# Kernel optimization log

Measured on AMD Instinct MI355X. Metric: run time of the kernel, lower is better.

Reference implementation:

```python
import jax, jax.numpy as jnp
import numpy as np

# Static configuration (mirrors TemporalAugmentation with deterministic choices)
B, T_IN, N, C = 32, 512, 543, 3
SPEED = 1.2                      # fixed draw from speed_range (0.8, 1.2)
NEW_T = int(T_IN / SPEED)        # 426
JITTER_FREQ = max(1, NEW_T // 8) # 53
FRAME_DROP_P = 0.1
JITTER_STD = 0.02
NOISE_STD = 0.01
SPATIAL_STD = 0.005


def linresample(x, out_T):
    """F.interpolate(mode='linear', align_corners=True) along last axis."""
    L = x.shape[-1]
    s = jnp.arange(out_T, dtype=x.dtype) * ((L - 1) / (out_T - 1))
    i0 = jnp.clip(jnp.floor(s).astype(jnp.int32), 0, L - 2)
    frac = s - i0.astype(x.dtype)
    return x[..., i0] * (1 - frac) + x[..., i0 + 1] * frac


def setup_inputs() -> dict:
    key = jax.random.key(0)
    k1, k2, k3, k4, k5 = jax.random.split(key, 5)
    x = jax.random.normal(k1, (B, T_IN, N, C), dtype=jnp.float32)
    mask = jnp.ones((B, T_IN), dtype=bool)
    keep_mask = jax.random.bernoulli(k2, 1.0 - FRAME_DROP_P, (B, NEW_T))
    keep_mask = keep_mask.at[:, 0].set(True).at[:, -1].set(True)
    base_jitter = jax.random.normal(k3, (B, JITTER_FREQ), dtype=jnp.float32)
    noise = jax.random.normal(k4, (B, NEW_T, N, C), dtype=jnp.float32)
    spatial_noise = jax.random.normal(k5, (B, 1, N, C), dtype=jnp.float32)
    return {"x": x, "mask": mask, "keep_mask": keep_mask,
            "base_jitter": base_jitter, "noise": noise,
            "spatial_noise": spatial_noise}


def reference(x, mask, keep_mask, base_jitter, noise, spatial_noise):
    Bb, T, Nn, Cc = x.shape
    # --- speed augment: linear resample time axis T -> NEW_T ---
    xt = jnp.moveaxis(x, 1, -1)                 # (B,N,C,T)
    x = jnp.moveaxis(linresample(xt, NEW_T), -1, 1)  # (B,NEW_T,N,C)
    # nearest resample of validity mask (PyTorch 'nearest': floor(t*in/out))
    nidx = jnp.floor(jnp.arange(NEW_T) * (T / NEW_T)).astype(jnp.int32)
    mask = mask[:, nidx]
    T2 = NEW_T
    # --- frame dropout: replace dropped frames with align_corners linear
    # resample of the kept-frame subsequence (length K) back to T2 ---
    K = keep_mask.sum(axis=1)                   # (B,) kept counts
    ar = jnp.arange(T2)
    # stable order putting kept indices first, in original order
    order = jnp.argsort(jnp.where(keep_mask, ar, T2 + ar), axis=1)  # (B,T2)
    s = ar[None, :].astype(x.dtype) * (K[:, None] - 1).astype(x.dtype) / (T2 - 1)
    r0 = jnp.clip(jnp.floor(s).astype(jnp.int32), 0, (K - 2)[:, None])
    frac = (s - r0.astype(x.dtype))[:, :, None, None]
    bidx = jnp.arange(Bb)[:, None]
    idx0 = jnp.take_along_axis(order, r0, axis=1)
    idx1 = jnp.take_along_axis(order, r0 + 1, axis=1)
    interp = x[bidx, idx0] * (1 - frac) + x[bidx, idx1] * frac
    x = jnp.where(keep_mask[:, :, None, None], x, interp)
    mask = mask & keep_mask
    # --- temporal jitter: scale per-frame velocity by smooth jitter curve ---
    jit = linresample(base_jitter * JITTER_STD, T2)   # (B,T2)
    vel = x[:, 1:] - x[:, :-1]
    x = jnp.concatenate([x[:, :1], x[:, 1:] + vel * jit[:, 1:, None, None]], axis=1)
    # --- coordinate noise + per-landmark spatial noise ---
    x = x + noise * NOISE_STD + spatial_noise * SPATIAL_STD
    return x, mask
```

## Files before the change

kernel.cpp:

```cpp
#include <hip/hip_runtime.h>
#include <stdint.h>

#define B_      32
#define T_IN_   512
#define N_      543
#define C_      3
#define NEW_T_  426
#define JF_     53
#define NC_     (N_*C_)
#define XOUT_   (B_*NEW_T_*NC_)
#define NGROUP_ (XOUT_/4)

#define MODE_INT   0
#define MODE_BYTE  1
#define MODE_FLOAT 2

__device__ __forceinline__ bool read_flag(const void* p, int mode, int idx) {
    if (mode == MODE_BYTE)  return ((const uint8_t*)p)[idx] != 0;
    if (mode == MODE_FLOAT) return ((const float*)p)[idx]   != 0.0f;
    return ((const int*)p)[idx] != 0;
}

__global__ __launch_bounds__(512) void prep_kernel(
    const void* __restrict__ maskp,
    const void* __restrict__ keepp,
    const float* __restrict__ bjit,
    float* __restrict__ out_mask,
    int4*  __restrict__ wsF,
    float4* __restrict__ wsW,
    float* __restrict__ wsJ)
{
    const int b = blockIdx.x;
    const int tid = threadIdx.x;

    __shared__ int flags[6];
    __shared__ int s_mode_mask, s_mode_keep;
    if (tid < 6) flags[tid] = 0;
    __syncthreads();
    if (tid < 64) {
        uint32_t vm = ((const uint32_t*)maskp)[tid];
        uint32_t vk = ((const uint32_t*)keepp)[tid];
        if (vm == 0x3F800000u)      atomicOr(&flags[2], 1);
        else if (vm > 1u)           atomicOr(&flags[1], 1);
        if (vk == 0x3F800000u)      atomicOr(&flags[5], 1);
        else if (vk > 1u)           atomicOr(&flags[4], 1);
    }
    __syncthreads();
    if (tid == 0) {
        s_mode_mask = flags[2] ? MODE_FLOAT : (flags[1] ? MODE_BYTE : MODE_INT);
        s_mode_keep = flags[5] ? MODE_FLOAT : (flags[4] ? MODE_BYTE : MODE_INT);
    }
    __syncthreads();
    const int mmode = s_mode_mask, kmode = s_mode_keep;

    __shared__ int sk[512];
    __shared__ int ps[512];
    __shared__ int kept[NEW_T_];

    int kv = 0;
    if (tid < NEW_T_) kv = read_flag(keepp, kmode, b*NEW_T_ + tid) ? 1 : 0;
    sk[tid] = (tid < NEW_T_) ? kv : 0;
    ps[tid] = sk[tid];
    __syncthreads();
    for (int off = 1; off < 512; off <<= 1) {
        int v = (tid >= off) ? ps[tid - off] : 0;
        __syncthreads();
        ps[tid] += v;
        __syncthreads();
    }
    const int K = ps[NEW_T_ - 1];
    if (tid < NEW_T_ && kv) kept[ps[tid] - 1] = tid;
    __syncthreads();

    if (tid < NEW_T_) {
        const int t = tid;
        const float RATX = (float)(511.0 / 425.0);
        float st = (float)t * RATX;
        int i0 = (int)floorf(st);
        if (i0 < 0) i0 = 0; if (i0 > T_IN_ - 2) i0 = T_IN_ - 2;
        float w = st - (float)i0;

        int4 F; float4 W;
        if (kv) {
            F = make_int4(i0, i0 + 1, 0, 1);
            W = make_float4(1.0f - w, w, 0.0f, 0.0f);
        } else {
            float s = ((float)t * (float)(K - 1)) / 425.0f;
            int r0 = (int)floorf(s);
            if (r0 < 0) r0 = 0; if (r0 > K - 2) r0 = K - 2;
            float f = s - (float)r0;
            int j0 = kept[r0], j1 = kept[r0 + 1];
            float s0 = (float)j0 * RATX;
            int a0 = (int)floorf(s0);
            if (a0 < 0) a0 = 0; if (a0 > T_IN_ - 2) a0 = T_IN_ - 2;
            float w0 = s0 - (float)a0;
            float s1 = (float)j1 * RATX;
            int a1 = (int)floorf(s1);
            if (a1 < 0) a1 = 0; if (a1 > T_IN_ - 2) a1 = T_IN_ - 2;
            float w1 = s1 - (float)a1;
            F = make_int4(a0, a0 + 1, a1, a1 + 1);
            W = make_float4((1.0f - f) * (1.0f - w0), (1.0f - f) * w0,
                            f * (1.0f - w1),          f * w1);
        }
        const int bt = b * NEW_T_ + t;
        wsF[bt] = F;
        wsW[bt] = W;

        const float RATJ = (float)(52.0 / 425.0);
        float sj = (float)t * RATJ;
        int ji = (int)floorf(sj);
        if (ji < 0) ji = 0; if (ji > JF_ - 2) ji = JF_ - 2;
        float jf = sj - (float)ji;
        float b0 = bjit[b*JF_ + ji]     * 0.02f;
        float b1 = bjit[b*JF_ + ji + 1] * 0.02f;
        float jv = b0 * (1.0f - jf) + b1 * jf;
        if (t == 0) jv = 0.0f;
        wsJ[bt] = jv;

        float mn = (float)t * (float)(512.0 / 426.0);
        int nidx = (int)floorf(mn);
        if (nidx > T_IN_ - 1) nidx = T_IN_ - 1;
        bool mo = read_flag(maskp, mmode, b*T_IN_ + nidx) && (kv != 0);
        out_mask[bt] = mo ? 1.0f : 0.0f;
    }
}

__global__ __launch_bounds__(256) void main_kernel(
    const float* __restrict__ x,
    const float* __restrict__ noise,
    const float* __restrict__ spat,
    const int4*  __restrict__ wsF,
    const float4* __restrict__ wsW,
    const float* __restrict__ wsJ,
    float* __restrict__ out)
{
    uint32_t g = blockIdx.x * 256u + threadIdx.x;
    if (g >= (uint32_t)NGROUP_) return;
    uint32_t flat = g * 4u;
    uint32_t bt = flat / (uint32_t)NC_;
    uint32_t e  = flat - bt * (uint32_t)NC_;

    if (e <= (uint32_t)(NC_ - 4)) {
        uint32_t b = bt / (uint32_t)NEW_T_;
        const float* xb = x + (size_t)b * (T_IN_ * NC_);
        int4  F  = wsF[bt];  float4 W  = wsW[bt];
        uint32_t pbt = bt ? bt - 1u : 0u;
        int4  FP = wsF[pbt]; float4 WP = wsW[pbt];
        float jv = wsJ[bt];

        const float* p0 = xb + (uint32_t)F.x * NC_ + e;
        const float* p1 = xb + (uint32_t)F.y * NC_ + e;
        const float* p2 = xb + (uint32_t)F.z * NC_ + e;
        const float* p3 = xb + (uint32_t)F.w * NC_ + e;
        const float* q0 = xb + (uint32_t)FP.x * NC_ + e;
        const float* q1 = xb + (uint32_t)FP.y * NC_ + e;
        const float* q2 = xb + (uint32_t)FP.z * NC_ + e;
        const float* q3 = xb + (uint32_t)FP.w * NC_ + e;

        float4 nz = *(const float4*)(noise + flat);
        const float* sp = spat + b * NC_ + e;

        float r[4];
        #pragma unroll
        for (int i = 0; i < 4; i++) {
            float a  = W.x  * p0[i] + W.y  * p1[i] + W.z  * p2[i] + W.w  * p3[i];
            float ap = WP.x * q0[i] + WP.y * q1[i] + WP.z * q2[i] + WP.w * q3[i];
            float nzv = (i == 0) ? nz.x : (i == 1) ? nz.y : (i == 2) ? nz.z : nz.w;
            r[i] = a + (a - ap) * jv + nzv * 0.01f + sp[i] * 0.005f;
        }
        float4 o; o.x = r[0]; o.y = r[1]; o.z = r[2]; o.w = r[3];
        *(float4*)(out + flat) = o;
    } else {
        #pragma unroll
        for (int i = 0; i < 4; i++) {
            uint32_t fl  = flat + i;
            uint32_t bt2 = fl / (uint32_t)NC_;
            uint32_t e2  = fl - bt2 * (uint32_t)NC_;
            uint32_t b2  = bt2 / (uint32_t)NEW_T_;
            const float* xb = x + (size_t)b2 * (T_IN_ * NC_);
            int4  F  = wsF[bt2];  float4 W  = wsW[bt2];
            uint32_t pbt = bt2 ? bt2 - 1u : 0u;
            int4  FP = wsF[pbt];  float4 WP = wsW[pbt];
            float jv = wsJ[bt2];
            float a  = W.x  * xb[(uint32_t)F.x  * NC_ + e2] + W.y  * xb[(uint32_t)F.y  * NC_ + e2]
                     + W.z  * xb[(uint32_t)F.z  * NC_ + e2] + W.w  * xb[(uint32_t)F.w  * NC_ + e2];
            float ap = WP.x * xb[(uint32_t)FP.x * NC_ + e2] + WP.y * xb[(uint32_t)FP.y * NC_ + e2]
                     + WP.z * xb[(uint32_t)FP.z * NC_ + e2] + WP.w * xb[(uint32_t)FP.w * NC_ + e2];
            out[fl] = a + (a - ap) * jv + noise[fl] * 0.01f + spat[b2 * NC_ + e2] * 0.005f;
        }
    }
}

extern "C" void kernel_launch(void* const* d_in, const int* in_sizes, int n_in,
                              void* d_out, int out_size, void* d_ws, size_t ws_size,
                              hipStream_t stream) {
    const float* x    = (const float*)d_in[0];
    const void*  mask = d_in[1];
    const void*  keep = d_in[2];
    const float* bjit = (const float*)d_in[3];
    const float* noise = (const float*)d_in[4];
    const float* spat  = (const float*)d_in[5];
    float* out = (float*)d_out;

    char* ws = (char*)d_ws;
    int4*   wsF = (int4*)ws;
    float4* wsW = (float4*)(ws + 218112);
    float*  wsJ = (float*)(ws + 436224);

    prep_kernel<<<B_, 512, 0, stream>>>(mask, keep, bjit,
                                        out + XOUT_, wsF, wsW, wsJ);
    const int nblk = (NGROUP_ + 255) / 256;
    main_kernel<<<nblk, 256, 0, stream>>>(x, noise, spat, wsF, wsW, wsJ, out);
}
```

Baseline: 278.0 us.

## Process frame chunks per block, reuse previous-frame interpolation, skip zero-weight taps

```diff
diff --git a/kernel.cpp b/kernel.cpp
--- a/kernel.cpp
+++ b/kernel.cpp
@@ -9,7 +9,8 @@
 #define JF_     53
 #define NC_     (N_*C_)
 #define XOUT_   (B_*NEW_T_*NC_)
-#define NGROUP_ (XOUT_/4)
+#define TF_     6
+#define NCH_    ((NEW_T_ + TF_ - 1) / TF_)
 
 #define MODE_INT   0
 #define MODE_BYTE  1
@@ -125,6 +126,27 @@
     }
 }
 
+__device__ __forceinline__ void compute_pd(float pd[7], const float* __restrict__ xb,
+                                           int4 F, float4 W, int tid) {
+    const float* p0 = xb + (uint32_t)F.x * NC_ + tid;
+    const float* p1 = xb + (uint32_t)F.y * NC_ + tid;
+    const bool four = (W.z != 0.0f) || (W.w != 0.0f);
+    if (four) {
+        const float* p2 = xb + (uint32_t)F.z * NC_ + tid;
+        const float* p3 = xb + (uint32_t)F.w * NC_ + tid;
+        #pragma unroll
+        for (int k = 0; k < 6; k++)
+            pd[k] = W.x * p0[256*k] + W.y * p1[256*k] + W.z * p2[256*k] + W.w * p3[256*k];
+        pd[6] = (tid < NC_ - 1536) ?
+            (W.x * p0[1536] + W.y * p1[1536] + W.z * p2[1536] + W.w * p3[1536]) : 0.0f;
+    } else {
+        #pragma unroll
+        for (int k = 0; k < 6; k++)
+            pd[k] = W.x * p0[256*k] + W.y * p1[256*k];
+        pd[6] = (tid < NC_ - 1536) ? (W.x * p0[1536] + W.y * p1[1536]) : 0.0f;
+    }
+}
+
 __global__ __launch_bounds__(256) void main_kernel(
     const float* __restrict__ x,
     const float* __restrict__ noise,
@@ -134,60 +156,49 @@
     const float* __restrict__ wsJ,
     float* __restrict__ out)
 {
-    uint32_t g = blockIdx.x * 256u + threadIdx.x;
-    if (g >= (uint32_t)NGROUP_) return;
-    uint32_t flat = g * 4u;
-    uint32_t bt = flat / (uint32_t)NC_;
-    uint32_t e  = flat - bt * (uint32_t)NC_;
-
-    if (e <= (uint32_t)(NC_ - 4)) {
-        uint32_t b = bt / (uint32_t)NEW_T_;
-        const float* xb = x + (size_t)b * (T_IN_ * NC_);
-        int4  F  = wsF[bt];  float4 W  = wsW[bt];
-        uint32_t pbt = bt ? bt - 1u : 0u;
-        int4  FP = wsF[pbt]; float4 WP = wsW[pbt];
+    const int b   = blockIdx.y;
+    const int t0  = blockIdx.x * TF_;
+    const int tid = threadIdx.x;
+    const float* xb = x + (size_t)b * (T_IN_ * NC_);
+
+    float sp[7];
+    {
+        const float* spb = spat + b * NC_ + tid;
+        #pragma unroll
+        for (int k = 0; k < 6; k++) sp[k] = spb[256*k];
+        sp[6] = (tid < NC_ - 1536) ? spb[1536] : 0.0f;
+    }
+
+    float pdp[7];
+    {
+        const int tp = (t0 > 0) ? (t0 - 1) : 0;
+        const int bt = b * NEW_T_ + tp;
+        int4 F = wsF[bt]; float4 W = wsW[bt];
+        compute_pd(pdp, xb, F, W, tid);
+    }
+
+    const int tend = (t0 + TF_ < NEW_T_) ? (t0 + TF_) : NEW_T_;
+    for (int t = t0; t < tend; t++) {
+        const int bt = b * NEW_T_ + t;
+        int4 F = wsF[bt]; float4 W = wsW[bt];
         float jv = wsJ[bt];
 
-        const float* p0 = xb + (uint32_t)F.x * NC_ + e;
-        const float* p1 = xb + (uint32_t)F.y * NC_ + e;
-        const float* p2 = xb + (uint32_t)F.z * NC_ + e;
-        const float* p3 = xb + (uint32_t)F.w * NC_ + e;
-        const float* q0 = xb + (uint32_t)FP.x * NC_ + e;
-        const float* q1 = xb + (uint32_t)FP.y * NC_ + e;
-        const float* q2 = xb + (uint32_t)FP.z * NC_ + e;
-        const float* q3 = xb + (uint32_t)FP.w * NC_ + e;
-
-        float4 nz = *(const float4*)(noise + flat);
-        const float* sp = spat + b * NC_ + e;
-
-        float r[4];
-        #pragma unroll
-        for (int i = 0; i < 4; i++) {
-            float a  = W.x  * p0[i] + W.y  * p1[i] + W.z  * p2[i] + W.w  * p3[i];
-            float ap = WP.x * q0[i] + WP.y * q1[i] + WP.z * q2[i] + WP.w * q3[i];
-            float nzv = (i == 0) ? nz.x : (i == 1) ? nz.y : (i == 2) ? nz.z : nz.w;
-            r[i] = a + (a - ap) * jv + nzv * 0.01f + sp[i] * 0.005f;
+        float pd[7];
+        compute_pd(pd, xb, F, W, tid);
+
+        const float* nz = noise + (size_t)bt * NC_ + tid;
+        float*       op = out   + (size_t)bt * NC_ + tid;
+        #pragma unroll
+        for (int k = 0; k < 6; k++) {
+            float r = pd[k] + (pd[k] - pdp[k]) * jv + nz[256*k] * 0.01f + sp[k] * 0.005f;
+            op[256*k] = r;
+            pdp[k] = pd[k];
         }
-        float4 o; o.x = r[0]; o.y = r[1]; o.z = r[2]; o.w = r[3];
-        *(float4*)(out + flat) = o;
-    } else {
-        #pragma unroll
-        for (int i = 0; i < 4; i++) {
-            uint32_t fl  = flat + i;
-            uint32_t bt2 = fl / (uint32_t)NC_;
-            uint32_t e2  = fl - bt2 * (uint32_t)NC_;
-            uint32_t b2  = bt2 / (uint32_t)NEW_T_;
-            const float* xb = x + (size_t)b2 * (T_IN_ * NC_);
-            int4  F  = wsF[bt2];  float4 W  = wsW[bt2];
-            uint32_t pbt = bt2 ? bt2 - 1u : 0u;
-            int4  FP = wsF[pbt];  float4 WP = wsW[pbt];
-            float jv = wsJ[bt2];
-            float a  = W.x  * xb[(uint32_t)F.x  * NC_ + e2] + W.y  * xb[(uint32_t)F.y  * NC_ + e2]
-                     + W.z  * xb[(uint32_t)F.z  * NC_ + e2] + W.w  * xb[(uint32_t)F.w  * NC_ + e2];
-            float ap = WP.x * xb[(uint32_t)FP.x * NC_ + e2] + WP.y * xb[(uint32_t)FP.y * NC_ + e2]
-                     + WP.z * xb[(uint32_t)FP.z * NC_ + e2] + WP.w * xb[(uint32_t)FP.w * NC_ + e2];
-            out[fl] = a + (a - ap) * jv + noise[fl] * 0.01f + spat[b2 * NC_ + e2] * 0.005f;
+        if (tid < NC_ - 1536) {
+            float r = pd[6] + (pd[6] - pdp[6]) * jv + nz[1536] * 0.01f + sp[6] * 0.005f;
+            op[1536] = r;
         }
+        pdp[6] = pd[6];
     }
 }
 
@@ -209,6 +220,6 @@
 
     prep_kernel<<<B_, 512, 0, stream>>>(mask, keep, bjit,
                                         out + XOUT_, wsF, wsW, wsJ);
-    const int nblk = (NGROUP_ + 255) / 256;
-    main_kernel<<<nblk, 256, 0, stream>>>(x, noise, spat, wsF, wsW, wsJ, out);
-}
+    dim3 grid(NCH_, B_);
+    main_kernel<<<grid, 256, 0, stream>>>(x, noise, spat, wsF, wsW, wsJ, out);
+}
```

After: 279.7 us. About the same (+0.6%).
